# Performance work log

Hardware: AMD Instinct MI355X
Metric: run time of the kernel (lower is better)

The kernel has to match this reference:

```python
import jax, jax.numpy as jnp
import numpy as np

S = 16384   # num src nodes
D = 16384   # num dst nodes
FS = 128    # src feature len
FD = 128    # dst feature len
R = 50.0    # dist threshold (m)
L = 2005.0  # box side so avg degree ~ 32
LN_EPS = 1e-5


def setup_inputs() -> dict:
    rng = np.random.default_rng(0)
    src_pos_np = rng.uniform(0.0, L, (S, 2)).astype(np.float32)
    dst_pos_np = rng.uniform(0.0, L, (D, 2)).astype(np.float32)
    # radius-graph edge construction (data-dependent, done once outside jit)
    es, ed = [], []
    CH = 2048
    for i in range(0, S, CH):
        d = np.linalg.norm(src_pos_np[i:i + CH, None, :] - dst_pos_np[None, :, :], axis=-1)
        si, di = np.nonzero(d <= R)
        es.append((si + i).astype(np.int32))
        ed.append(di.astype(np.int32))
    edge_src_idx = jnp.asarray(np.concatenate(es))
    edge_dst_idx = jnp.asarray(np.concatenate(ed))

    key = jax.random.key(0)
    ks = jax.random.split(key, 12)
    w = lambda k, shape: (jax.random.normal(k, shape, jnp.float32) * 0.02)
    return {
        'src_node_features': jax.random.normal(ks[0], (S, FS), jnp.float32),
        'src_node_pos': jnp.asarray(src_pos_np),
        'dst_node_features': jax.random.normal(ks[1], (D, FD), jnp.float32),
        'dst_node_pos': jnp.asarray(dst_pos_np),
        'src_w': w(ks[2], (FS, FS)), 'src_b': jnp.zeros((FS,), jnp.float32),
        'dst_w': w(ks[3], (FD, FD)), 'dst_b': jnp.zeros((FD,), jnp.float32),
        'dist_w': w(ks[4], (2, FD)), 'dist_b': jnp.zeros((FD,), jnp.float32),
        'edge_w1': w(ks[5], (FS + FD + FD, FD)), 'edge_b1': jnp.zeros((FD,), jnp.float32),
        'edge_w2': w(ks[6], (FD, FD)), 'edge_b2': jnp.zeros((FD,), jnp.float32),
        'ln_g': jnp.ones((FD,), jnp.float32), 'ln_b': jnp.zeros((FD,), jnp.float32),
        'out_w': w(ks[7], (FD, FD)), 'out_b': jnp.zeros((FD,), jnp.float32),
        'edge_src_idx': edge_src_idx,
        'edge_dst_idx': edge_dst_idx,
    }


def reference(src_node_features, src_node_pos, dst_node_features, dst_node_pos,
              src_w, src_b, dst_w, dst_b, dist_w, dist_b,
              edge_w1, edge_b1, edge_w2, edge_b2, ln_g, ln_b, out_w, out_b,
              edge_src_idx, edge_dst_idx):
    # node encoders: Linear + ReLU
    src_enc = jax.nn.relu(src_node_features @ src_w + src_b)   # [S, FS]
    dst_enc = jax.nn.relu(dst_node_features @ dst_w + dst_b)   # [D, FD]
    # gather per-edge
    e_src = src_enc[edge_src_idx]                               # [E, FS]
    e_dst = dst_enc[edge_dst_idx]                               # [E, FD]
    e_dpos = src_node_pos[edge_src_idx] - dst_node_pos[edge_dst_idx]  # [E, 2]
    e_dist = jax.nn.relu(e_dpos @ dist_w + dist_b)              # [E, FD]
    # edge MLP: Linear-ReLU-Linear on concat [E, FS+FD+FD]
    e_in = jnp.concatenate([e_src, e_dist, e_dst], axis=-1)
    e_out = jax.nn.relu(e_in @ edge_w1 + edge_b1) @ edge_w2 + edge_b2  # [E, FD]
    # scatter-add to destination nodes
    agg = dst_enc + jax.ops.segment_sum(e_out, edge_dst_idx, num_segments=D)
    # LayerNorm + ReLU + Linear + residual + ReLU
    mu = jnp.mean(agg, axis=-1, keepdims=True)
    var = jnp.mean(jnp.square(agg - mu), axis=-1, keepdims=True)
    ln = (agg - mu) * jax.lax.rsqrt(var + LN_EPS) * ln_g + ln_b
    h = jax.nn.relu(ln) @ out_w + out_b + dst_node_features
    return jax.nn.relu(h)
```

## Files before the change

kernel.cpp:

```cpp
#include <hip/hip_runtime.h>

typedef unsigned short ushort_t;
typedef unsigned int uint_t;
typedef short bhalf8 __attribute__((ext_vector_type(8)));
typedef float f32x4 __attribute__((ext_vector_type(4)));

__device__ __forceinline__ float b2f(ushort_t u) {
    union { uint_t i; float f; } v; v.i = ((uint_t)u) << 16; return v.f;
}
__device__ __forceinline__ float u2f(uint_t u) {
    union { uint_t i; float f; } v; v.i = u; return v.f;
}
__device__ __forceinline__ ushort_t f2b(float f) {
    union { float f; uint_t i; } v; v.f = f;
    uint_t r = v.i + 0x7fffu + ((v.i >> 16) & 1u);
    return (ushort_t)(r >> 16);
}
__device__ __forceinline__ uint_t f2u(float f) {
    union { float f; uint_t i; } v; v.f = f; return v.i;
}
__device__ __forceinline__ uint_t pack_trunc(float lo, float hi) {
    return (f2u(lo) >> 16) | (f2u(hi) & 0xffff0000u);
}
__device__ __forceinline__ uint_t addpack_trunc(uint_t a, uint_t b) {
    union { uint_t i; float f; } t0, t1, s0, s1;
    t0.i = a << 16;          s0.i = b << 16;
    t1.i = a & 0xffff0000u;  s1.i = b & 0xffff0000u;
    return pack_trunc(t0.f + s0.f, t1.f + s1.f);
}

__global__ __launch_bounds__(256) void prep_kernel(
    const float* __restrict__ wsrc, const float* __restrict__ wdst,
    const float* __restrict__ w2,   const float* __restrict__ wout,
    const float* __restrict__ w1,
    ushort_t* __restrict__ msrc, ushort_t* __restrict__ mdst,
    ushort_t* __restrict__ m2,   ushort_t* __restrict__ mout,
    ushort_t* __restrict__ m1a,  ushort_t* __restrict__ m1b,
    ushort_t* __restrict__ m1c,
    const int* __restrict__ edi, int E, int* __restrict__ deg,
    float* __restrict__ hsum, int countB, int zeroB, int Dn)
{
    int b = blockIdx.x, tid = threadIdx.x;
    if (b < 56) {
        const float* ins[7] = { wsrc, wdst, w2, wout, w1, w1 + 128*128, w1 + 256*128 };
        ushort_t* outs[7]   = { msrc, mdst, m2, mout, m1a, m1b, m1c };
        int mat = b >> 3;
        const float* in = ins[mat];
        ushort_t* out = outs[mat];
        int flat = (b & 7)*256 + tid;
        int nt = flat >> 8, rem = flat & 255;
        int ks = rem >> 6, lane = rem & 63;
        int q = lane >> 4, m = lane & 15;
        #pragma unroll
        for (int j = 0; j < 8; ++j)
            out[flat*8 + j] = f2b(in[(ks*32 + q*8 + j)*128 + nt*16 + m]);
    } else if (b < 56 + countB) {
        int i = (b - 56)*256 + tid;
        if (i < E) atomicAdd(&deg[edi[i]], 1);
    } else {
        int zb = b - 56 - countB;
        float4* h4 = (float4*)hsum;
        int total4 = Dn*32;
        for (int i = zb*256 + tid; i < total4; i += zeroB*256)
            h4[i] = make_float4(0.f, 0.f, 0.f, 0.f);
    }
}

__global__ __launch_bounds__(256) void enc2_kernel(
    const float* __restrict__ src_feat, const float* __restrict__ dst_feat,
    const ushort_t* __restrict__ msrc, const ushort_t* __restrict__ mdst,
    const ushort_t* __restrict__ m1a,  const ushort_t* __restrict__ m1c,
    const float* __restrict__ src_b,   const float* __restrict__ dst_b,
    const float* __restrict__ b1,
    ushort_t* __restrict__ Csrc, ushort_t* __restrict__ Cdst,
    ushort_t* __restrict__ dst_enc,
    const int* __restrict__ deg, int* __restrict__ nxt, int Dn,
    int Sb, int Db)
{
    int tid = threadIdx.x, blk = blockIdx.x;

    if (blk == Sb + Db) {
        __shared__ int sums[256];
        int per = Dn >> 8;
        const int4* d4 = (const int4*)(deg + tid*per);
        int4 v[16]; int s = 0;
        #pragma unroll
        for (int k = 0; k < 16; ++k) { v[k] = d4[k]; s += v[k].x + v[k].y + v[k].z + v[k].w; }
        sums[tid] = s;
        __syncthreads();
        for (int off = 1; off < 256; off <<= 1) {
            int x = (tid >= off) ? sums[tid - off] : 0;
            __syncthreads();
            sums[tid] += x;
            __syncthreads();
        }
        int run = sums[tid] - s;
        int4* n4 = (int4*)(nxt + tid*per);
        #pragma unroll
        for (int k = 0; k < 16; ++k) {
            int4 o;
            o.x = run; run += v[k].x;
            o.y = run; run += v[k].y;
            o.z = run; run += v[k].z;
            o.w = run; run += v[k].w;
            n4[k] = o;
        }
        return;
    }

    __shared__ ushort_t A_l[64*136];
    __shared__ ushort_t E_l[64*136];
    __shared__ float b_l[128];
    __shared__ float b2_l[128];

    const float* A; const ushort_t *W1m, *W2m; const float* bias;
    ushort_t *outC, *outEnc; int rowbase; const float* bias2;
    if (blk < Sb) { A = src_feat; W1m = msrc; W2m = m1a; bias = src_b;
                    outC = Csrc; outEnc = nullptr; rowbase = blk*64; bias2 = nullptr; }
    else          { A = dst_feat; W1m = mdst; W2m = m1c; bias = dst_b;
                    outC = Cdst; outEnc = dst_enc; rowbase = (blk - Sb)*64; bias2 = b1; }

    const float4* A4 = (const float4*)A;
    for (int i = tid; i < 2048; i += 256) {
        int r = i >> 5, c = i & 31;
        float4 v = A4[(size_t)(rowbase + r)*32 + c];
        uint2 u;
        u.x = pack_trunc(v.x, v.y);
        u.y = pack_trunc(v.z, v.w);
        *(uint2*)(A_l + r*136 + c*4) = u;
    }
    if (tid < 128) { b_l[tid] = bias[tid]; b2_l[tid] = bias2 ? bias2[tid] : 0.f; }
    __syncthreads();

    int lane = tid & 63, w = tid >> 6, q = lane >> 4, m = lane & 15;
    const bhalf8* Wv1 = (const bhalf8*)W1m;
    f32x4 acc[4][2] = {};
    #pragma unroll
    for (int ks = 0; ks < 4; ++ks) {
        bhalf8 bf0 = Wv1[((2*w)*4 + ks)*64 + lane];
        bhalf8 bf1 = Wv1[((2*w+1)*4 + ks)*64 + lane];
        #pragma unroll
        for (int mt = 0; mt < 4; ++mt) {
            bhalf8 a = *(const bhalf8*)(A_l + (mt*16 + m)*136 + ks*32 + q*8);
            acc[mt][0] = __builtin_amdgcn_mfma_f32_16x16x32_bf16(a, bf0, acc[mt][0], 0, 0, 0);
            acc[mt][1] = __builtin_amdgcn_mfma_f32_16x16x32_bf16(a, bf1, acc[mt][1], 0, 0, 0);
        }
    }
    #pragma unroll
    for (int mt = 0; mt < 4; ++mt)
    #pragma unroll
    for (int nt = 0; nt < 2; ++nt)
    #pragma unroll
    for (int reg = 0; reg < 4; ++reg) {
        int col = w*32 + nt*16 + m;
        int row = mt*16 + q*4 + reg;
        E_l[row*136 + col] = f2b(fmaxf(acc[mt][nt][reg] + b_l[col], 0.f));
    }
    __syncthreads();

    if (outEnc) {
        for (int i = tid; i < 1024; i += 256) {
            int r = i >> 4, c = i & 15;
            ((uint4*)outEnc)[(size_t)(rowbase + r)*16 + c] = *(const uint4*)(E_l + r*136 + c*8);
        }
    }

    const bhalf8* Wv2 = (const bhalf8*)W2m;
    f32x4 acc2[4][2] = {};
    #pragma unroll
    for (int ks = 0; ks < 4; ++ks) {
        bhalf8 bf0 = Wv2[((2*w)*4 + ks)*64 + lane];
        bhalf8 bf1 = Wv2[((2*w+1)*4 + ks)*64 + lane];
        #pragma unroll
        for (int mt = 0; mt < 4; ++mt) {
            bhalf8 a = *(const bhalf8*)(E_l + (mt*16 + m)*136 + ks*32 + q*8);
            acc2[mt][0] = __builtin_amdgcn_mfma_f32_16x16x32_bf16(a, bf0, acc2[mt][0], 0, 0, 0);
            acc2[mt][1] = __builtin_amdgcn_mfma_f32_16x16x32_bf16(a, bf1, acc2[mt][1], 0, 0, 0);
        }
    }
    #pragma unroll
    for (int mt = 0; mt < 4; ++mt)
    #pragma unroll
    for (int nt = 0; nt < 2; ++nt)
    #pragma unroll
    for (int reg = 0; reg < 4; ++reg) {
        int col = w*32 + nt*16 + m;
        int row = mt*16 + q*4 + reg;
        A_l[row*136 + col] = f2b(acc2[mt][nt][reg] + b2_l[col]);
    }
    __syncthreads();
    for (int i = tid; i < 1024; i += 256) {
        int r = i >> 4, c = i & 15;
        ((uint4*)outC)[(size_t)(rowbase + r)*16 + c] = *(const uint4*)(A_l + r*136 + c*8);
    }
}

__global__ __launch_bounds__(256) void fill_sorted(
    const int* __restrict__ esi, const int* __restrict__ edi, int E,
    int* __restrict__ nxt, int2* __restrict__ spair)
{
    int i = blockIdx.x*256 + threadIdx.x;
    if (i < E) {
        int s = esi[i], d = edi[i];
        int p = atomicAdd(&nxt[d], 1);
        spair[p] = make_int2(s, d);
    }
}

__global__ __launch_bounds__(256, 4) void edge_kernel(
    const ushort_t* __restrict__ Csrc, const ushort_t* __restrict__ Cdst,
    const float* __restrict__ src_pos, const float* __restrict__ dst_pos,
    const int2* __restrict__ spair, int E,
    const ushort_t* __restrict__ w1bm,
    const float* __restrict__ dist_w, const float* __restrict__ dist_b,
    float* __restrict__ hsum)
{
    __shared__ char pool[17408];
    __shared__ ushort_t G[64*136];
    __shared__ int s_l[64], d_l[64], dofs_l[64];
    __shared__ uint_t bndmask[2];
    __shared__ float dx_l[64], dy_l[64];
    __shared__ float dw0_l[128], dw1_l[128], db_l[128];

    ushort_t* X  = (ushort_t*)pool;
    ushort_t* Hc = (ushort_t*)pool;

    int tid = threadIdx.x, blk = blockIdx.x;

    if (tid < 64) {
        int slot = blk*64 + tid;
        int s = 0, d = -1;
        float dx = 0.f, dy = 0.f;
        if (slot < E) {
            int2 pr = spair[slot];
            s = pr.x; d = pr.y;
            float2 sp = ((const float2*)src_pos)[s];
            float2 dp = ((const float2*)dst_pos)[d];
            dx = sp.x - dp.x; dy = sp.y - dp.y;
        }
        s_l[tid] = s; d_l[tid] = d;
        dofs_l[tid] = (d >= 0) ? d*128 : -1;
        dx_l[tid] = dx; dy_l[tid] = dy;
    }
    if (tid < 128) {
        dw0_l[tid] = dist_w[tid];
        dw1_l[tid] = dist_w[128 + tid];
        db_l[tid]  = dist_b[tid];
    }
    __syncthreads();

    if (tid < 64) {
        int d = d_l[tid];
        int dn = (tid < 63) ? d_l[tid + 1] : -2;
        bool bnd = (tid == 31) || (tid == 63) || (dn != d);
        unsigned long long mask = __ballot(bnd);
        if (tid == 0) { bndmask[0] = (uint_t)mask; bndmask[1] = (uint_t)(mask >> 32); }
    }

    const uint4* cs4 = (const uint4*)Csrc;
    const uint4* cd4 = (const uint4*)Cdst;
    #pragma unroll
    for (int k = 0; k < 4; ++k) {
        int i = tid + k*256;
        int r = i >> 4, c = i & 15;
        uint4 a = cs4[(size_t)s_l[r]*16 + c];
        uint4 b = cd4[(size_t)max(d_l[r], 0)*16 + c];
        uint4 u;
        u.x = addpack_trunc(a.x, b.x);
        u.y = addpack_trunc(a.y, b.y);
        u.z = addpack_trunc(a.z, b.z);
        u.w = addpack_trunc(a.w, b.w);
        *(uint4*)(G + r*136 + c*8) = u;
    }
    for (int i = tid; i < 4096; i += 256) {
        int r = i >> 6, j2 = (i & 63)*2;
        float dx = dx_l[r], dy = dy_l[r];
        float v0 = fmaxf(fmaf(dx, dw0_l[j2],   fmaf(dy, dw1_l[j2],   db_l[j2])),   0.f);
        float v1 = fmaxf(fmaf(dx, dw0_l[j2+1], fmaf(dy, dw1_l[j2+1], db_l[j2+1])), 0.f);
        *(uint_t*)(X + r*136 + j2) = pack_trunc(v0, v1);
    }
    __syncthreads();

    int lane = tid & 63, w = tid >> 6, q = lane >> 4, m = lane & 15;
    f32x4 acc[4][2] = {};
    const bhalf8* Wv = (const bhalf8*)w1bm;
    #pragma unroll
    for (int ks = 0; ks < 4; ++ks) {
        bhalf8 bf0 = Wv[((2*w)*4 + ks)*64 + lane];
        bhalf8 bf1 = Wv[((2*w+1)*4 + ks)*64 + lane];
        #pragma unroll
        for (int mt = 0; mt < 4; ++mt) {
            bhalf8 a = *(const bhalf8*)(X + (mt*16 + m)*136 + ks*32 + q*8);
            acc[mt][0] = __builtin_amdgcn_mfma_f32_16x16x32_bf16(a, bf0, acc[mt][0], 0, 0, 0);
            acc[mt][1] = __builtin_amdgcn_mfma_f32_16x16x32_bf16(a, bf1, acc[mt][1], 0, 0, 0);
        }
    }
    __syncthreads();

    #pragma unroll
    for (int mt = 0; mt < 4; ++mt)
    #pragma unroll
    for (int nt = 0; nt < 2; ++nt) {
        int col = w*32 + nt*16 + m;
        int row0 = mt*16 + q*4;
        uint2 u;
        u.x = pack_trunc(acc[mt][nt][0], acc[mt][nt][1]);
        u.y = pack_trunc(acc[mt][nt][2], acc[mt][nt][3]);
        *(uint2*)(Hc + col*68 + row0) = u;
    }
    __syncthreads();

    {
        int j = tid & 127, h = tid >> 7;
        uint_t mask = bndmask[h];
        const ushort_t* Hcol = Hc + j*68 + h*32;
        int rbase = h*32;
        float a = 0.f;
        #pragma unroll
        for (int k8 = 0; k8 < 8; ++k8) {
            uint2 hp = *(const uint2*)(Hcol + k8*4);
            float hv[4];
            hv[0] = u2f(hp.x << 16);
            hv[1] = u2f(hp.x & 0xffff0000u);
            hv[2] = u2f(hp.y << 16);
            hv[3] = u2f(hp.y & 0xffff0000u);
            #pragma unroll
            for (int t = 0; t < 4; ++t) {
                int r = rbase + k8*4 + t;
                float g = b2f(G[r*136 + j]);
                a += fmaxf(hv[t] + g, 0.f);
                if ((mask >> (k8*4 + t)) & 1u) {
                    int ofs = dofs_l[r];
                    if (ofs >= 0) atomicAdd(&hsum[(size_t)ofs + j], a);
                    a = 0.f;
                }
            }
        }
    }
}

__global__ __launch_bounds__(256) void aggfinal_kernel(
    const float* __restrict__ hsum, const ushort_t* __restrict__ w2m,
    const float* __restrict__ b2, const int* __restrict__ deg,
    const ushort_t* __restrict__ dst_enc, const float* __restrict__ ln_g,
    const float* __restrict__ ln_b, const ushort_t* __restrict__ moutm,
    const float* __restrict__ out_b, const float* __restrict__ dst_feat,
    float* __restrict__ out)
{
    __shared__ char buf[64*132*4];
    __shared__ ushort_t act_l[64*136];
    __shared__ float b2_l[128], g_l[128], bl_l[128], ob_l[128];
    __shared__ int deg_l[64];
    __shared__ float ps[64][4], ps2[64][4], mu_l[64], inv_l[64];

    ushort_t* A_l = (ushort_t*)buf;
    float* Y = (float*)buf;
    int tid = threadIdx.x, blk = blockIdx.x;

    const float4* hv = (const float4*)hsum;
    for (int i = tid; i < 1024; i += 256) {
        int r = i >> 4, c = i & 15;
        size_t base = (size_t)(blk*64 + r)*32 + c*2;
        float4 p0 = hv[base], p1 = hv[base + 1];
        uint4 u;
        u.x = pack_trunc(p0.x, p0.y);
        u.y = pack_trunc(p0.z, p0.w);
        u.z = pack_trunc(p1.x, p1.y);
        u.w = pack_trunc(p1.z, p1.w);
        *(uint4*)(A_l + r*136 + c*8) = u;
    }
    if (tid < 128) { b2_l[tid] = b2[tid]; g_l[tid] = ln_g[tid];
                     bl_l[tid] = ln_b[tid]; ob_l[tid] = out_b[tid]; }
    if (tid < 64) deg_l[tid] = deg[blk*64 + tid];
    __syncthreads();

    int lane = tid & 63, w = tid >> 6, q = lane >> 4, m = lane & 15;
    f32x4 acc[4][2] = {};
    const bhalf8* Wv = (const bhalf8*)w2m;
    #pragma unroll
    for (int ks = 0; ks < 4; ++ks) {
        bhalf8 bf0 = Wv[((2*w)*4 + ks)*64 + lane];
        bhalf8 bf1 = Wv[((2*w+1)*4 + ks)*64 + lane];
        #pragma unroll
        for (int mt = 0; mt < 4; ++mt) {
            bhalf8 a = *(const bhalf8*)(A_l + (mt*16 + m)*136 + ks*32 + q*8);
            acc[mt][0] = __builtin_amdgcn_mfma_f32_16x16x32_bf16(a, bf0, acc[mt][0], 0, 0, 0);
            acc[mt][1] = __builtin_amdgcn_mfma_f32_16x16x32_bf16(a, bf1, acc[mt][1], 0, 0, 0);
        }
    }
    __syncthreads();

    #pragma unroll
    for (int mt = 0; mt < 4; ++mt)
    #pragma unroll
    for (int nt = 0; nt < 2; ++nt)
    #pragma unroll
    for (int reg = 0; reg < 4; ++reg) {
        int col = w*32 + nt*16 + m;
        int rowl = mt*16 + q*4 + reg;
        size_t grow = (size_t)blk*64 + rowl;
        float v = acc[mt][nt][reg] + (float)deg_l[rowl]*b2_l[col] + b2f(dst_enc[grow*128 + col]);
        Y[rowl*132 + col] = v;
    }
    __syncthreads();

    {
        int r = tid >> 2, t4 = tid & 3;
        float s = 0.f, s2 = 0.f;
        for (int jj = 0; jj < 32; ++jj) {
            float v = Y[r*132 + t4*32 + jj];
            s += v; s2 += v*v;
        }
        ps[r][t4] = s; ps2[r][t4] = s2;
    }
    __syncthreads();
    if (tid < 64) {
        int r = tid;
        float sum = ps[r][0] + ps[r][1] + ps[r][2] + ps[r][3];
        float sum2 = ps2[r][0] + ps2[r][1] + ps2[r][2] + ps2[r][3];
        float mu = sum / 128.f;
        float var = sum2 / 128.f - mu*mu;
        mu_l[r] = mu;
        inv_l[r] = 1.0f / sqrtf(var + 1e-5f);
    }
    __syncthreads();
    for (int i = tid; i < 4096; i += 256) {
        int r = i >> 6, j2 = (i & 63)*2;
        float v0 = fmaxf((Y[r*132 + j2]   - mu_l[r]) * inv_l[r] * g_l[j2]   + bl_l[j2],   0.f);
        float v1 = fmaxf((Y[r*132 + j2+1] - mu_l[r]) * inv_l[r] * g_l[j2+1] + bl_l[j2+1], 0.f);
        *(uint_t*)(act_l + r*136 + j2) = (uint_t)f2b(v0) | ((uint_t)f2b(v1) << 16);
    }
    __syncthreads();

    f32x4 acc2[4][2] = {};
    const bhalf8* Wo = (const bhalf8*)moutm;
    #pragma unroll
    for (int ks = 0; ks < 4; ++ks) {
        bhalf8 bf0 = Wo[((2*w)*4 + ks)*64 + lane];
        bhalf8 bf1 = Wo[((2*w+1)*4 + ks)*64 + lane];
        #pragma unroll
        for (int mt = 0; mt < 4; ++mt) {
            bhalf8 a = *(const bhalf8*)(act_l + (mt*16 + m)*136 + ks*32 + q*8);
            acc2[mt][0] = __builtin_amdgcn_mfma_f32_16x16x32_bf16(a, bf0, acc2[mt][0], 0, 0, 0);
            acc2[mt][1] = __builtin_amdgcn_mfma_f32_16x16x32_bf16(a, bf1, acc2[mt][1], 0, 0, 0);
        }
    }
    #pragma unroll
    for (int mt = 0; mt < 4; ++mt)
    #pragma unroll
    for (int nt = 0; nt < 2; ++nt)
    #pragma unroll
    for (int reg = 0; reg < 4; ++reg) {
        int col = w*32 + nt*16 + m;
        size_t row = (size_t)blk*64 + mt*16 + q*4 + reg;
        float v = acc2[mt][nt][reg] + ob_l[col] + dst_feat[row*128 + col];
        out[row*128 + col] = fmaxf(v, 0.f);
    }
}

extern "C" void kernel_launch(void* const* d_in, const int* in_sizes, int n_in,
                              void* d_out, int out_size, void* d_ws, size_t ws_size,
                              hipStream_t stream)
{
    const float* src_feat = (const float*)d_in[0];
    const float* src_pos  = (const float*)d_in[1];
    const float* dst_feat = (const float*)d_in[2];
    const float* dst_pos  = (const float*)d_in[3];
    const float* src_w    = (const float*)d_in[4];
    const float* src_b    = (const float*)d_in[5];
    const float* dst_w    = (const float*)d_in[6];
    const float* dst_b    = (const float*)d_in[7];
    const float* dist_w   = (const float*)d_in[8];
    const float* dist_b   = (const float*)d_in[9];
    const float* w1       = (const float*)d_in[10];
    const float* b1       = (const float*)d_in[11];
    const float* w2       = (const float*)d_in[12];
    const float* b2       = (const float*)d_in[13];
    const float* ln_g     = (const float*)d_in[14];
    const float* ln_b     = (const float*)d_in[15];
    const float* out_w    = (const float*)d_in[16];
    const float* out_b    = (const float*)d_in[17];
    const int* esi        = (const int*)d_in[18];
    const int* edi        = (const int*)d_in[19];
    int E = in_sizes[18];
    int S = in_sizes[0] / 128;
    int D = in_sizes[2] / 128;

    char* ws = (char*)d_ws;
    size_t off = 0;
    auto alloc = [&](size_t bytes) { char* p = ws + off; off += (bytes + 511) & ~(size_t)511; return p; };
    ushort_t* Csrc    = (ushort_t*)alloc((size_t)S*128*2);
    ushort_t* Cdst    = (ushort_t*)alloc((size_t)D*128*2);
    ushort_t* dst_enc = (ushort_t*)alloc((size_t)D*128*2);
    float*    hsum    = (float*)   alloc((size_t)D*128*4);
    ushort_t* msrc    = (ushort_t*)alloc(128*128*2);
    ushort_t* mdst    = (ushort_t*)alloc(128*128*2);
    ushort_t* m2      = (ushort_t*)alloc(128*128*2);
    ushort_t* mout    = (ushort_t*)alloc(128*128*2);
    ushort_t* m1a     = (ushort_t*)alloc(128*128*2);
    ushort_t* m1b     = (ushort_t*)alloc(128*128*2);
    ushort_t* m1c     = (ushort_t*)alloc(128*128*2);
    int*      deg     = (int*)     alloc((size_t)D*4);
    int*      nxt     = (int*)     alloc((size_t)D*4);
    int2*     spair   = (int2*)    alloc((size_t)E*8);

    hipMemsetAsync(deg, 0, (size_t)D*4, stream);

    int countB = (E + 255)/256;
    int zeroB = 256;
    prep_kernel<<<56 + countB + zeroB, 256, 0, stream>>>(
        src_w, dst_w, w2, out_w, w1,
        msrc, mdst, m2, mout, m1a, m1b, m1c,
        edi, E, deg, hsum, countB, zeroB, D);

    int Sb = S/64, Db = D/64;
    enc2_kernel<<<Sb + Db + 1, 256, 0, stream>>>(
        src_feat, dst_feat, msrc, mdst, m1a, m1c, src_b, dst_b, b1,
        Csrc, Cdst, dst_enc, deg, nxt, D, Sb, Db);

    fill_sorted<<<(E + 255)/256, 256, 0, stream>>>(esi, edi, E, nxt, spair);

    edge_kernel<<<(E + 63)/64, 256, 0, stream>>>(
        Csrc, Cdst, src_pos, dst_pos, spair, E,
        m1b, dist_w, dist_b, hsum);

    aggfinal_kernel<<<Db, 256, 0, stream>>>(
        hsum, m2, b2, deg, dst_enc, ln_g, ln_b,
        mout, out_b, dst_feat, (float*)d_out);
}
```

Before: 224.6 us.

## Fuse all stages into one cooperative persistent kernel with grid syncs

```diff
diff --git a/kernel.cpp b/kernel.cpp
--- a/kernel.cpp
+++ b/kernel.cpp
@@ -1,4 +1,7 @@
 #include <hip/hip_runtime.h>
+#include <hip/hip_cooperative_groups.h>
+
+namespace cg = cooperative_groups;
 
 typedef unsigned short ushort_t;
 typedef unsigned int uint_t;
@@ -27,6 +30,428 @@
     t0.i = a << 16;          s0.i = b << 16;
     t1.i = a & 0xffff0000u;  s1.i = b & 0xffff0000u;
     return pack_trunc(t0.f + s0.f, t1.f + s1.f);
+}
+
+__global__ __launch_bounds__(256, 3) void gnn_mega(
+    const float* __restrict__ src_feat, const float* __restrict__ dst_feat,
+    const float* __restrict__ src_pos,  const float* __restrict__ dst_pos,
+    const float* __restrict__ wsrc, const float* __restrict__ src_b,
+    const float* __restrict__ wdst, const float* __restrict__ dst_b,
+    const float* __restrict__ dist_w, const float* __restrict__ dist_b,
+    const float* __restrict__ w1, const float* __restrict__ b1,
+    const float* __restrict__ w2g, const float* __restrict__ b2g,
+    const float* __restrict__ ln_g, const float* __restrict__ ln_b,
+    const float* __restrict__ woutg, const float* __restrict__ out_bg,
+    const int* __restrict__ esi, const int* __restrict__ edi, int E,
+    ushort_t* __restrict__ t_src, ushort_t* __restrict__ t_dst,
+    ushort_t* __restrict__ t_w2,  ushort_t* __restrict__ t_out,
+    ushort_t* __restrict__ t_1a,  ushort_t* __restrict__ t_1b,
+    ushort_t* __restrict__ t_1c,
+    ushort_t* __restrict__ Csrc, ushort_t* __restrict__ Cdst,
+    ushort_t* __restrict__ dst_enc,
+    float* __restrict__ hsum, int* __restrict__ deg, int* __restrict__ nxt,
+    int2* __restrict__ spair, float* __restrict__ out, int S, int D)
+{
+    __shared__ __align__(16) char smem[37648];
+    int tid = threadIdx.x, blk = blockIdx.x, nB = gridDim.x;
+    int lane = tid & 63, w = tid >> 6, q = lane >> 4, m = lane & 15;
+    cg::grid_group grid = cg::this_grid();
+
+    if (blk < 56) {
+        const float* ins[7] = { wsrc, wdst, w2g, woutg, w1, w1 + 16384, w1 + 32768 };
+        ushort_t* outs[7]   = { t_src, t_dst, t_w2, t_out, t_1a, t_1b, t_1c };
+        int mat = blk >> 3;
+        int flat = (blk & 7)*256 + tid;
+        int nt = flat >> 8, rem = flat & 255;
+        int ks = rem >> 6, l2 = rem & 63;
+        int qq = l2 >> 4, mm = l2 & 15;
+        const float* in = ins[mat];
+        ushort_t* o = outs[mat];
+        #pragma unroll
+        for (int j = 0; j < 8; ++j)
+            o[flat*8 + j] = f2b(in[(ks*32 + qq*8 + j)*128 + nt*16 + mm]);
+    }
+    for (int i = blk*256 + tid; i < E; i += nB*256) atomicAdd(&deg[edi[i]], 1);
+    {
+        float4 z = make_float4(0.f, 0.f, 0.f, 0.f);
+        float4* h4 = (float4*)hsum;
+        int tot = D*32;
+        for (int i = blk*256 + tid; i < tot; i += nB*256) h4[i] = z;
+    }
+    grid.sync();
+
+    int Sb = S/64, Db = D/64;
+    for (int vb = blk; vb < Sb + Db; vb += nB) {
+        ushort_t* A_l = (ushort_t*)smem;
+        ushort_t* E_l = (ushort_t*)(smem + 17408);
+        float* b_l  = (float*)(smem + 34816);
+        float* pb2  = (float*)(smem + 35328);
+
+        const float* A; const ushort_t *W1m, *W2m; const float* bias; const float* bias2;
+        ushort_t *outC, *outEnc; int rowbase;
+        if (vb < Sb) { A = src_feat; W1m = t_src; W2m = t_1a; bias = src_b;
+                       outC = Csrc; outEnc = nullptr; rowbase = vb*64; bias2 = nullptr; }
+        else         { A = dst_feat; W1m = t_dst; W2m = t_1c; bias = dst_b;
+                       outC = Cdst; outEnc = dst_enc; rowbase = (vb - Sb)*64; bias2 = b1; }
+
+        const float4* A4 = (const float4*)A;
+        for (int i = tid; i < 2048; i += 256) {
+            int r = i >> 5, c = i & 31;
+            float4 v = A4[(size_t)(rowbase + r)*32 + c];
+            uint2 u;
+            u.x = pack_trunc(v.x, v.y);
+            u.y = pack_trunc(v.z, v.w);
+            *(uint2*)(A_l + r*136 + c*4) = u;
+        }
+        if (tid < 128) { b_l[tid] = bias[tid]; pb2[tid] = bias2 ? bias2[tid] : 0.f; }
+        __syncthreads();
+
+        const bhalf8* Wv1 = (const bhalf8*)W1m;
+        f32x4 acc[4][2] = {};
+        #pragma unroll
+        for (int ks = 0; ks < 4; ++ks) {
+            bhalf8 bf0 = Wv1[((2*w)*4 + ks)*64 + lane];
+            bhalf8 bf1 = Wv1[((2*w+1)*4 + ks)*64 + lane];
+            #pragma unroll
+            for (int mt = 0; mt < 4; ++mt) {
+                bhalf8 a = *(const bhalf8*)(A_l + (mt*16 + m)*136 + ks*32 + q*8);
+                acc[mt][0] = __builtin_amdgcn_mfma_f32_16x16x32_bf16(a, bf0, acc[mt][0], 0, 0, 0);
+                acc[mt][1] = __builtin_amdgcn_mfma_f32_16x16x32_bf16(a, bf1, acc[mt][1], 0, 0, 0);
+            }
+        }
+        #pragma unroll
+        for (int mt = 0; mt < 4; ++mt)
+        #pragma unroll
+        for (int nt = 0; nt < 2; ++nt)
+        #pragma unroll
+        for (int reg = 0; reg < 4; ++reg) {
+            int col = w*32 + nt*16 + m;
+            int row = mt*16 + q*4 + reg;
+            E_l[row*136 + col] = f2b(fmaxf(acc[mt][nt][reg] + b_l[col], 0.f));
+        }
+        __syncthreads();
+
+        if (outEnc) {
+            for (int i = tid; i < 1024; i += 256) {
+                int r = i >> 4, c = i & 15;
+                ((uint4*)outEnc)[(size_t)(rowbase + r)*16 + c] = *(const uint4*)(E_l + r*136 + c*8);
+            }
+        }
+
+        const bhalf8* Wv2 = (const bhalf8*)W2m;
+        f32x4 acc2[4][2] = {};
+        #pragma unroll
+        for (int ks = 0; ks < 4; ++ks) {
+            bhalf8 bf0 = Wv2[((2*w)*4 + ks)*64 + lane];
+            bhalf8 bf1 = Wv2[((2*w+1)*4 + ks)*64 + lane];
+            #pragma unroll
+            for (int mt = 0; mt < 4; ++mt) {
+                bhalf8 a = *(const bhalf8*)(E_l + (mt*16 + m)*136 + ks*32 + q*8);
+                acc2[mt][0] = __builtin_amdgcn_mfma_f32_16x16x32_bf16(a, bf0, acc2[mt][0], 0, 0, 0);
+                acc2[mt][1] = __builtin_amdgcn_mfma_f32_16x16x32_bf16(a, bf1, acc2[mt][1], 0, 0, 0);
+            }
+        }
+        #pragma unroll
+        for (int mt = 0; mt < 4; ++mt)
+        #pragma unroll
+        for (int nt = 0; nt < 2; ++nt)
+        #pragma unroll
+        for (int reg = 0; reg < 4; ++reg) {
+            int col = w*32 + nt*16 + m;
+            int row = mt*16 + q*4 + reg;
+            A_l[row*136 + col] = f2b(acc2[mt][nt][reg] + pb2[col]);
+        }
+        __syncthreads();
+        for (int i = tid; i < 1024; i += 256) {
+            int r = i >> 4, c = i & 15;
+            ((uint4*)outC)[(size_t)(rowbase + r)*16 + c] = *(const uint4*)(A_l + r*136 + c*8);
+        }
+        __syncthreads();
+    }
+    if (blk == nB - 1) {
+        int* sums = (int*)(smem + 36608);
+        int per = D >> 8;
+        const int4* d4 = (const int4*)(deg + tid*per);
+        int s = 0;
+        for (int k = 0; k < per/4; ++k) { int4 v = d4[k]; s += v.x + v.y + v.z + v.w; }
+        sums[tid] = s;
+        __syncthreads();
+        for (int off = 1; off < 256; off <<= 1) {
+            int x = (tid >= off) ? sums[tid - off] : 0;
+            __syncthreads();
+            sums[tid] += x;
+            __syncthreads();
+        }
+        int run = sums[tid] - s;
+        int4* n4 = (int4*)(nxt + tid*per);
+        for (int k = 0; k < per/4; ++k) {
+            int4 v = d4[k];
+            int4 o;
+            o.x = run; run += v.x;
+            o.y = run; run += v.y;
+            o.z = run; run += v.z;
+            o.w = run; run += v.w;
+            n4[k] = o;
+        }
+    }
+    grid.sync();
+
+    for (int i = blk*256 + tid; i < E; i += nB*256) {
+        int s = esi[i], d = edi[i];
+        int p = atomicAdd(&nxt[d], 1);
+        spair[p] = make_int2(s, d);
+    }
+    grid.sync();
+
+    {
+        ushort_t* X   = (ushort_t*)smem;
+        ushort_t* G   = (ushort_t*)(smem + 17408);
+        float* dw0    = (float*)(smem + 34816);
+        float* dw1    = (float*)(smem + 35328);
+        float* dbv    = (float*)(smem + 35840);
+        int* s_l      = (int*)(smem + 36352);
+        int* d_l      = (int*)(smem + 36608);
+        int* dofs     = (int*)(smem + 36864);
+        float* dx_l   = (float*)(smem + 37120);
+        float* dy_l   = (float*)(smem + 37376);
+        uint_t* bnd   = (uint_t*)(smem + 37632);
+
+        if (tid < 128) {
+            dw0[tid] = dist_w[tid];
+            dw1[tid] = dist_w[128 + tid];
+            dbv[tid] = dist_b[tid];
+        }
+        const bhalf8* Wv = (const bhalf8*)t_1b;
+        bhalf8 wf0[4], wf1[4];
+        #pragma unroll
+        for (int ks = 0; ks < 4; ++ks) {
+            wf0[ks] = Wv[((2*w)*4 + ks)*64 + lane];
+            wf1[ks] = Wv[((2*w+1)*4 + ks)*64 + lane];
+        }
+
+        int nT = (E + 63) >> 6;
+        for (int tile = blk; tile < nT; tile += nB) {
+            __syncthreads();
+            if (tid < 64) {
+                int slot = tile*64 + tid;
+                int s = 0, d = -1;
+                float dx = 0.f, dy = 0.f;
+                if (slot < E) {
+                    int2 pr = spair[slot];
+                    s = pr.x; d = pr.y;
+                    float2 sp = ((const float2*)src_pos)[s];
+                    float2 dp = ((const float2*)dst_pos)[d];
+                    dx = sp.x - dp.x; dy = sp.y - dp.y;
+                }
+                s_l[tid] = s; d_l[tid] = d;
+                dofs[tid] = (d >= 0) ? d*128 : -1;
+                dx_l[tid] = dx; dy_l[tid] = dy;
+            }
+            __syncthreads();
+            if (tid < 64) {
+                int d = d_l[tid];
+                int dn = (tid < 63) ? d_l[tid + 1] : -2;
+                bool bb = (tid == 31) || (tid == 63) || (dn != d);
+                unsigned long long mask = __ballot(bb);
+                if (tid == 0) { bnd[0] = (uint_t)mask; bnd[1] = (uint_t)(mask >> 32); }
+            }
+            const uint4* cs4 = (const uint4*)Csrc;
+            const uint4* cd4 = (const uint4*)Cdst;
+            #pragma unroll
+            for (int k = 0; k < 4; ++k) {
+                int i = tid + k*256;
+                int r = i >> 4, c = i & 15;
+                uint4 a = cs4[(size_t)s_l[r]*16 + c];
+                uint4 b = cd4[(size_t)max(d_l[r], 0)*16 + c];
+                uint4 u;
+                u.x = addpack_trunc(a.x, b.x);
+                u.y = addpack_trunc(a.y, b.y);
+                u.z = addpack_trunc(a.z, b.z);
+                u.w = addpack_trunc(a.w, b.w);
+                *(uint4*)(G + r*136 + c*8) = u;
+            }
+            for (int i = tid; i < 4096; i += 256) {
+                int r = i >> 6, j2 = (i & 63)*2;
+                float dx = dx_l[r], dy = dy_l[r];
+                float v0 = fmaxf(fmaf(dx, dw0[j2],   fmaf(dy, dw1[j2],   dbv[j2])),   0.f);
+                float v1 = fmaxf(fmaf(dx, dw0[j2+1], fmaf(dy, dw1[j2+1], dbv[j2+1])), 0.f);
+                *(uint_t*)(X + r*136 + j2) = pack_trunc(v0, v1);
+            }
+            __syncthreads();
+
+            f32x4 acc[4][2] = {};
+            #pragma unroll
+            for (int ks = 0; ks < 4; ++ks) {
+                #pragma unroll
+                for (int mt = 0; mt < 4; ++mt) {
+                    bhalf8 a = *(const bhalf8*)(X + (mt*16 + m)*136 + ks*32 + q*8);
+                    acc[mt][0] = __builtin_amdgcn_mfma_f32_16x16x32_bf16(a, wf0[ks], acc[mt][0], 0, 0, 0);
+                    acc[mt][1] = __builtin_amdgcn_mfma_f32_16x16x32_bf16(a, wf1[ks], acc[mt][1], 0, 0, 0);
+                }
+            }
+            __syncthreads();
+
+            ushort_t* Hc = X;
+            #pragma unroll
+            for (int mt = 0; mt < 4; ++mt)
+            #pragma unroll
+            for (int nt = 0; nt < 2; ++nt) {
+                int col = w*32 + nt*16 + m;
+                int row0 = mt*16 + q*4;
+                uint2 u;
+                u.x = pack_trunc(acc[mt][nt][0], acc[mt][nt][1]);
+                u.y = pack_trunc(acc[mt][nt][2], acc[mt][nt][3]);
+                *(uint2*)(Hc + col*68 + row0) = u;
+            }
+            __syncthreads();
+
+            {
+                int j = tid & 127, h = tid >> 7;
+                uint_t mask = bnd[h];
+                const ushort_t* Hcol = Hc + j*68 + h*32;
+                int rbase = h*32;
+                float a = 0.f;
+                #pragma unroll
+                for (int k8 = 0; k8 < 8; ++k8) {
+                    uint2 hp = *(const uint2*)(Hcol + k8*4);
+                    float hv[4];
+                    hv[0] = u2f(hp.x << 16);
+                    hv[1] = u2f(hp.x & 0xffff0000u);
+                    hv[2] = u2f(hp.y << 16);
+                    hv[3] = u2f(hp.y & 0xffff0000u);
+                    #pragma unroll
+                    for (int t = 0; t < 4; ++t) {
+                        int r = rbase + k8*4 + t;
+                        float g = b2f(G[r*136 + j]);
+                        a += fmaxf(hv[t] + g, 0.f);
+                        if ((mask >> (k8*4 + t)) & 1u) {
+                            int ofs = dofs[r];
+                            if (ofs >= 0) atomicAdd(&hsum[(size_t)ofs + j], a);
+                            a = 0.f;
+                        }
+                    }
+                }
+            }
+        }
+    }
+    grid.sync();
+
+    {
+        ushort_t* A_l = (ushort_t*)smem;
+        ushort_t* E2  = (ushort_t*)(smem + 4352);
+        float* ps   = (float*)(smem + 8704);
+        float* ps2  = (float*)(smem + 8960);
+        float* muv  = (float*)(smem + 9216);
+        float* invv = (float*)(smem + 9280);
+        float* pb2  = (float*)(smem + 9344);
+        float* pg   = (float*)(smem + 9856);
+        float* plb  = (float*)(smem + 10368);
+        float* pob  = (float*)(smem + 10880);
+        int*   dgl  = (int*)(smem + 11392);
+
+        int nT4 = D >> 4;
+        for (int t4 = blk; t4 < nT4; t4 += nB) {
+            __syncthreads();
+            if (tid < 128) { pb2[tid] = b2g[tid]; pg[tid] = ln_g[tid];
+                             plb[tid] = ln_b[tid]; pob[tid] = out_bg[tid]; }
+            if (tid < 16) dgl[tid] = deg[t4*16 + tid];
+            {
+                int r = tid >> 4, c = tid & 15;
+                const float4* hv4 = (const float4*)hsum;
+                size_t base = (size_t)(t4*16 + r)*32 + c*2;
+                float4 p0 = hv4[base], p1 = hv4[base + 1];
+                uint4 u;
+                u.x = pack_trunc(p0.x, p0.y);
+                u.y = pack_trunc(p0.z, p0.w);
+                u.z = pack_trunc(p1.x, p1.y);
+                u.w = pack_trunc(p1.z, p1.w);
+                *(uint4*)(A_l + r*136 + c*8) = u;
+                *(uint4*)(E2 + r*136 + c*8) = ((const uint4*)dst_enc)[(size_t)(t4*16 + r)*16 + c];
+            }
+            __syncthreads();
+
+            const bhalf8* Wv2 = (const bhalf8*)t_w2;
+            f32x4 acc[2] = {};
+            #pragma unroll
+            for (int ks = 0; ks < 4; ++ks) {
+                bhalf8 bf0 = Wv2[((2*w)*4 + ks)*64 + lane];
+                bhalf8 bf1 = Wv2[((2*w+1)*4 + ks)*64 + lane];
+                bhalf8 a = *(const bhalf8*)(A_l + m*136 + ks*32 + q*8);
+                acc[0] = __builtin_amdgcn_mfma_f32_16x16x32_bf16(a, bf0, acc[0], 0, 0, 0);
+                acc[1] = __builtin_amdgcn_mfma_f32_16x16x32_bf16(a, bf1, acc[1], 0, 0, 0);
+            }
+            float y[2][4];
+            #pragma unroll
+            for (int nt = 0; nt < 2; ++nt)
+            #pragma unroll
+            for (int reg = 0; reg < 4; ++reg) {
+                int col = w*32 + nt*16 + m;
+                int rowl = q*4 + reg;
+                y[nt][reg] = acc[nt][reg] + (float)dgl[rowl]*pb2[col] + b2f(E2[rowl*136 + col]);
+            }
+            float s[4], s2[4];
+            #pragma unroll
+            for (int reg = 0; reg < 4; ++reg) {
+                s[reg]  = y[0][reg] + y[1][reg];
+                s2[reg] = y[0][reg]*y[0][reg] + y[1][reg]*y[1][reg];
+            }
+            #pragma unroll
+            for (int o = 1; o < 16; o <<= 1) {
+                #pragma unroll
+                for (int reg = 0; reg < 4; ++reg) {
+                    s[reg]  += __shfl_xor(s[reg],  o);
+                    s2[reg] += __shfl_xor(s2[reg], o);
+                }
+            }
+            if (m == 0) {
+                #pragma unroll
+                for (int reg = 0; reg < 4; ++reg) {
+                    ps[(q*4 + reg)*4 + w]  = s[reg];
+                    ps2[(q*4 + reg)*4 + w] = s2[reg];
+                }
+            }
+            __syncthreads();
+            if (tid < 16) {
+                float su = ps[tid*4] + ps[tid*4+1] + ps[tid*4+2] + ps[tid*4+3];
+                float sq = ps2[tid*4] + ps2[tid*4+1] + ps2[tid*4+2] + ps2[tid*4+3];
+                float mu = su / 128.f;
+                float var = sq / 128.f - mu*mu;
+                muv[tid] = mu;
+                invv[tid] = 1.0f / sqrtf(var + 1e-5f);
+            }
+            __syncthreads();
+            #pragma unroll
+            for (int nt = 0; nt < 2; ++nt)
+            #pragma unroll
+            for (int reg = 0; reg < 4; ++reg) {
+                int col = w*32 + nt*16 + m;
+                int rowl = q*4 + reg;
+                float v = (y[nt][reg] - muv[rowl])*invv[rowl]*pg[col] + plb[col];
+                A_l[rowl*136 + col] = f2b(fmaxf(v, 0.f));
+            }
+            __syncthreads();
+
+            const bhalf8* Wo = (const bhalf8*)t_out;
+            f32x4 acc2[2] = {};
+            #pragma unroll
+            for (int ks = 0; ks < 4; ++ks) {
+                bhalf8 bf0 = Wo[((2*w)*4 + ks)*64 + lane];
+                bhalf8 bf1 = Wo[((2*w+1)*4 + ks)*64 + lane];
+                bhalf8 a = *(const bhalf8*)(A_l + m*136 + ks*32 + q*8);
+                acc2[0] = __builtin_amdgcn_mfma_f32_16x16x32_bf16(a, bf0, acc2[0], 0, 0, 0);
+                acc2[1] = __builtin_amdgcn_mfma_f32_16x16x32_bf16(a, bf1, acc2[1], 0, 0, 0);
+            }
+            #pragma unroll
+            for (int nt = 0; nt < 2; ++nt)
+            #pragma unroll
+            for (int reg = 0; reg < 4; ++reg) {
+                int col = w*32 + nt*16 + m;
+                size_t grow = (size_t)t4*16 + q*4 + reg;
+                float v = acc2[nt][reg] + pob[col] + dst_feat[grow*128 + col];
+                out[grow*128 + col] = fmaxf(v, 0.f);
+            }
+        }
+    }
 }
 
 __global__ __launch_bounds__(256) void prep_kernel(
@@ -42,7 +467,7 @@
 {
     int b = blockIdx.x, tid = threadIdx.x;
     if (b < 56) {
-        const float* ins[7] = { wsrc, wdst, w2, wout, w1, w1 + 128*128, w1 + 256*128 };
+        const float* ins[7] = { wsrc, wdst, w2, wout, w1, w1 + 16384, w1 + 32768 };
         ushort_t* outs[7]   = { msrc, mdst, m2, mout, m1a, m1b, m1c };
         int mat = b >> 3;
         const float* in = ins[mat];
@@ -113,8 +538,8 @@
     __shared__ float b_l[128];
     __shared__ float b2_l[128];
 
-    const float* A; const ushort_t *W1m, *W2m; const float* bias;
-    ushort_t *outC, *outEnc; int rowbase; const float* bias2;
+    const float* A; const ushort_t *W1m, *W2m; const float* bias; const float* bias2;
+    ushort_t *outC, *outEnc; int rowbase;
     if (blk < Sb) { A = src_feat; W1m = msrc; W2m = m1a; bias = src_b;
                     outC = Csrc; outEnc = nullptr; rowbase = blk*64; bias2 = nullptr; }
     else          { A = dst_feat; W1m = mdst; W2m = m1c; bias = dst_b;
@@ -493,38 +918,51 @@
     ushort_t* Cdst    = (ushort_t*)alloc((size_t)D*128*2);
     ushort_t* dst_enc = (ushort_t*)alloc((size_t)D*128*2);
     float*    hsum    = (float*)   alloc((size_t)D*128*4);
-    ushort_t* msrc    = (ushort_t*)alloc(128*128*2);
-    ushort_t* mdst    = (ushort_t*)alloc(128*128*2);
-    ushort_t* m2      = (ushort_t*)alloc(128*128*2);
-    ushort_t* mout    = (ushort_t*)alloc(128*128*2);
-    ushort_t* m1a     = (ushort_t*)alloc(128*128*2);
-    ushort_t* m1b     = (ushort_t*)alloc(128*128*2);
-    ushort_t* m1c     = (ushort_t*)alloc(128*128*2);
+    ushort_t* t_src   = (ushort_t*)alloc(128*128*2);
+    ushort_t* t_dst   = (ushort_t*)alloc(128*128*2);
+    ushort_t* t_w2    = (ushort_t*)alloc(128*128*2);
+    ushort_t* t_out   = (ushort_t*)alloc(128*128*2);
+    ushort_t* t_1a    = (ushort_t*)alloc(128*128*2);
+    ushort_t* t_1b    = (ushort_t*)alloc(128*128*2);
+    ushort_t* t_1c    = (ushort_t*)alloc(128*128*2);
     int*      deg     = (int*)     alloc((size_t)D*4);
     int*      nxt     = (int*)     alloc((size_t)D*4);
     int2*     spair   = (int2*)    alloc((size_t)E*8);
+    float*    outp    = (float*)d_out;
 
     hipMemsetAsync(deg, 0, (size_t)D*4, stream);
 
-    int countB = (E + 255)/256;
-    int zeroB = 256;
-    prep_kernel<<<56 + countB + zeroB, 256, 0, stream>>>(
-        src_w, dst_w, w2, out_w, w1,
-        msrc, mdst, m2, mout, m1a, m1b, m1c,
-        edi, E, deg, hsum, countB, zeroB, D);
-
-    int Sb = S/64, Db = D/64;
-    enc2_kernel<<<Sb + Db + 1, 256, 0, stream>>>(
-        src_feat, dst_feat, msrc, mdst, m1a, m1c, src_b, dst_b, b1,
-        Csrc, Cdst, dst_enc, deg, nxt, D, Sb, Db);
-
-    fill_sorted<<<(E + 255)/256, 256, 0, stream>>>(esi, edi, E, nxt, spair);
-
-    edge_kernel<<<(E + 63)/64, 256, 0, stream>>>(
-        Csrc, Cdst, src_pos, dst_pos, spair, E,
-        m1b, dist_w, dist_b, hsum);
-
-    aggfinal_kernel<<<Db, 256, 0, stream>>>(
-        hsum, m2, b2, deg, dst_enc, ln_g, ln_b,
-        mout, out_b, dst_feat, (float*)d_out);
-}
+    void* args[] = {
+        (void*)&src_feat, (void*)&dst_feat, (void*)&src_pos, (void*)&dst_pos,
+        (void*)&src_w, (void*)&src_b, (void*)&dst_w, (void*)&dst_b,
+        (void*)&dist_w, (void*)&dist_b, (void*)&w1, (void*)&b1,
+        (void*)&w2, (void*)&b2, (void*)&ln_g, (void*)&ln_b,
+        (void*)&out_w, (void*)&out_b, (void*)&esi, (void*)&edi, (void*)&E,
+        (void*)&t_src, (void*)&t_dst, (void*)&t_w2, (void*)&t_out,
+        (void*)&t_1a, (void*)&t_1b, (void*)&t_1c,
+        (void*)&Csrc, (void*)&Cdst, (void*)&dst_enc,
+        (void*)&hsum, (void*)&deg, (void*)&nxt, (void*)&spair,
+        (void*)&outp, (void*)&S, (void*)&D
+    };
+    hipError_t rc = hipLaunchCooperativeKernel((void*)gnn_mega, dim3(768), dim3(256),
+                                               args, 0, stream);
+    if (rc != hipSuccess) {
+        int countB = (E + 255)/256;
+        int zeroB = 256;
+        prep_kernel<<<56 + countB + zeroB, 256, 0, stream>>>(
+            src_w, dst_w, w2, out_w, w1,
+            t_src, t_dst, t_w2, t_out, t_1a, t_1b, t_1c,
+            edi, E, deg, hsum, countB, zeroB, D);
+        int Sb = S/64, Db = D/64;
+        enc2_kernel<<<Sb + Db + 1, 256, 0, stream>>>(
+            src_feat, dst_feat, t_src, t_dst, t_1a, t_1c, src_b, dst_b, b1,
+            Csrc, Cdst, dst_enc, deg, nxt, D, Sb, Db);
+        fill_sorted<<<(E + 255)/256, 256, 0, stream>>>(esi, edi, E, nxt, spair);
+        edge_kernel<<<(E + 63)/64, 256, 0, stream>>>(
+            Csrc, Cdst, src_pos, dst_pos, spair, E,
+            t_1b, dist_w, dist_b, hsum);
+        aggfinal_kernel<<<Db, 256, 0, stream>>>(
+            hsum, t_w2, b2, deg, dst_enc, ln_g, ln_b,
+            t_out, out_b, dst_feat, outp);
+    }
+}
```

Result: slower. 623.2 us (+177.5%).

## Shrink final aggregation kernel to 16-row blocks with shuffle-based LayerNorm

Applied to the files above, without the earlier changes.

```diff
diff --git a/kernel.cpp b/kernel.cpp
--- a/kernel.cpp
+++ b/kernel.cpp
@@ -42,7 +42,7 @@
 {
     int b = blockIdx.x, tid = threadIdx.x;
     if (b < 56) {
-        const float* ins[7] = { wsrc, wdst, w2, wout, w1, w1 + 128*128, w1 + 256*128 };
+        const float* ins[7] = { wsrc, wdst, w2, wout, w1, w1 + 16384, w1 + 32768 };
         ushort_t* outs[7]   = { msrc, mdst, m2, mout, m1a, m1b, m1c };
         int mat = b >> 3;
         const float* in = ins[mat];
@@ -113,8 +113,8 @@
     __shared__ float b_l[128];
     __shared__ float b2_l[128];
 
-    const float* A; const ushort_t *W1m, *W2m; const float* bias;
-    ushort_t *outC, *outEnc; int rowbase; const float* bias2;
+    const float* A; const ushort_t *W1m, *W2m; const float* bias; const float* bias2;
+    ushort_t *outC, *outEnc; int rowbase;
     if (blk < Sb) { A = src_feat; W1m = msrc; W2m = m1a; bias = src_b;
                     outC = Csrc; outEnc = nullptr; rowbase = blk*64; bias2 = nullptr; }
     else          { A = dst_feat; W1m = mdst; W2m = m1c; bias = dst_b;
@@ -339,7 +339,7 @@
     }
 }
 
-__global__ __launch_bounds__(256) void aggfinal_kernel(
+__global__ __launch_bounds__(256) void aggfinal16_kernel(
     const float* __restrict__ hsum, const ushort_t* __restrict__ w2m,
     const float* __restrict__ b2, const int* __restrict__ deg,
     const ushort_t* __restrict__ dst_enc, const float* __restrict__ ln_g,
@@ -347,114 +347,113 @@
     const float* __restrict__ out_b, const float* __restrict__ dst_feat,
     float* __restrict__ out)
 {
-    __shared__ char buf[64*132*4];
-    __shared__ ushort_t act_l[64*136];
-    __shared__ float b2_l[128], g_l[128], bl_l[128], ob_l[128];
-    __shared__ int deg_l[64];
-    __shared__ float ps[64][4], ps2[64][4], mu_l[64], inv_l[64];
-
-    ushort_t* A_l = (ushort_t*)buf;
-    float* Y = (float*)buf;
+    __shared__ ushort_t A_l[16*136];
+    __shared__ ushort_t E2[16*136];
+    __shared__ float ps[64], ps2[64];
+    __shared__ float muv[16], invv[16];
+    __shared__ float pb2[128], pg[128], plb[128], pob[128];
+    __shared__ int dgl[16];
+
     int tid = threadIdx.x, blk = blockIdx.x;
-
-    const float4* hv = (const float4*)hsum;
-    for (int i = tid; i < 1024; i += 256) {
-        int r = i >> 4, c = i & 15;
-        size_t base = (size_t)(blk*64 + r)*32 + c*2;
-        float4 p0 = hv[base], p1 = hv[base + 1];
+    int lane = tid & 63, w = tid >> 6, q = lane >> 4, m = lane & 15;
+
+    if (tid < 128) { pb2[tid] = b2[tid]; pg[tid] = ln_g[tid];
+                     plb[tid] = ln_b[tid]; pob[tid] = out_b[tid]; }
+    if (tid < 16) dgl[tid] = deg[blk*16 + tid];
+    {
+        int r = tid >> 4, c = tid & 15;
+        const float4* hv4 = (const float4*)hsum;
+        size_t base = (size_t)(blk*16 + r)*32 + c*2;
+        float4 p0 = hv4[base], p1 = hv4[base + 1];
         uint4 u;
         u.x = pack_trunc(p0.x, p0.y);
         u.y = pack_trunc(p0.z, p0.w);
         u.z = pack_trunc(p1.x, p1.y);
         u.w = pack_trunc(p1.z, p1.w);
         *(uint4*)(A_l + r*136 + c*8) = u;
-    }
-    if (tid < 128) { b2_l[tid] = b2[tid]; g_l[tid] = ln_g[tid];
-                     bl_l[tid] = ln_b[tid]; ob_l[tid] = out_b[tid]; }
-    if (tid < 64) deg_l[tid] = deg[blk*64 + tid];
-    __syncthreads();
-
-    int lane = tid & 63, w = tid >> 6, q = lane >> 4, m = lane & 15;
-    f32x4 acc[4][2] = {};
-    const bhalf8* Wv = (const bhalf8*)w2m;
+        *(uint4*)(E2 + r*136 + c*8) = ((const uint4*)dst_enc)[(size_t)(blk*16 + r)*16 + c];
+    }
+    __syncthreads();
+
+    const bhalf8* Wv2 = (const bhalf8*)w2m;
+    f32x4 acc[2] = {};
     #pragma unroll
     for (int ks = 0; ks < 4; ++ks) {
-        bhalf8 bf0 = Wv[((2*w)*4 + ks)*64 + lane];
-        bhalf8 bf1 = Wv[((2*w+1)*4 + ks)*64 + lane];
-        #pragma unroll
-        for (int mt = 0; mt < 4; ++mt) {
-            bhalf8 a = *(const bhalf8*)(A_l + (mt*16 + m)*136 + ks*32 + q*8);
-            acc[mt][0] = __builtin_amdgcn_mfma_f32_16x16x32_bf16(a, bf0, acc[mt][0], 0, 0, 0);
-            acc[mt][1] = __builtin_amdgcn_mfma_f32_16x16x32_bf16(a, bf1, acc[mt][1], 0, 0, 0);
-        }
-    }
-    __syncthreads();
-
-    #pragma unroll
-    for (int mt = 0; mt < 4; ++mt)
+        bhalf8 bf0 = Wv2[((2*w)*4 + ks)*64 + lane];
+        bhalf8 bf1 = Wv2[((2*w+1)*4 + ks)*64 + lane];
+        bhalf8 a = *(const bhalf8*)(A_l + m*136 + ks*32 + q*8);
+        acc[0] = __builtin_amdgcn_mfma_f32_16x16x32_bf16(a, bf0, acc[0], 0, 0, 0);
+        acc[1] = __builtin_amdgcn_mfma_f32_16x16x32_bf16(a, bf1, acc[1], 0, 0, 0);
+    }
+    float y[2][4];
     #pragma unroll
     for (int nt = 0; nt < 2; ++nt)
     #pragma unroll
     for (int reg = 0; reg < 4; ++reg) {
         int col = w*32 + nt*16 + m;
-        int rowl = mt*16 + q*4 + reg;
-        size_t grow = (size_t)blk*64 + rowl;
-        float v = acc[mt][nt][reg] + (float)deg_l[rowl]*b2_l[col] + b2f(dst_enc[grow*128 + col]);
-        Y[rowl*132 + col] = v;
-    }
-    __syncthreads();
-
-    {
-        int r = tid >> 2, t4 = tid & 3;
-        float s = 0.f, s2 = 0.f;
-        for (int jj = 0; jj < 32; ++jj) {
-            float v = Y[r*132 + t4*32 + jj];
-            s += v; s2 += v*v;
-        }
-        ps[r][t4] = s; ps2[r][t4] = s2;
-    }
-    __syncthreads();
-    if (tid < 64) {
-        int r = tid;
-        float sum = ps[r][0] + ps[r][1] + ps[r][2] + ps[r][3];
-        float sum2 = ps2[r][0] + ps2[r][1] + ps2[r][2] + ps2[r][3];
-        float mu = sum / 128.f;
-        float var = sum2 / 128.f - mu*mu;
-        mu_l[r] = mu;
-        inv_l[r] = 1.0f / sqrtf(var + 1e-5f);
-    }
-    __syncthreads();
-    for (int i = tid; i < 4096; i += 256) {
-        int r = i >> 6, j2 = (i & 63)*2;
-        float v0 = fmaxf((Y[r*132 + j2]   - mu_l[r]) * inv_l[r] * g_l[j2]   + bl_l[j2],   0.f);
-        float v1 = fmaxf((Y[r*132 + j2+1] - mu_l[r]) * inv_l[r] * g_l[j2+1] + bl_l[j2+1], 0.f);
-        *(uint_t*)(act_l + r*136 + j2) = (uint_t)f2b(v0) | ((uint_t)f2b(v1) << 16);
-    }
-    __syncthreads();
-
-    f32x4 acc2[4][2] = {};
+        int rowl = q*4 + reg;
+        y[nt][reg] = acc[nt][reg] + (float)dgl[rowl]*pb2[col] + b2f(E2[rowl*136 + col]);
+    }
+    float s[4], s2[4];
+    #pragma unroll
+    for (int reg = 0; reg < 4; ++reg) {
+        s[reg]  = y[0][reg] + y[1][reg];
+        s2[reg] = y[0][reg]*y[0][reg] + y[1][reg]*y[1][reg];
+    }
+    #pragma unroll
+    for (int o = 1; o < 16; o <<= 1) {
+        #pragma unroll
+        for (int reg = 0; reg < 4; ++reg) {
+            s[reg]  += __shfl_xor(s[reg],  o);
+            s2[reg] += __shfl_xor(s2[reg], o);
+        }
+    }
+    if (m == 0) {
+        #pragma unroll
+        for (int reg = 0; reg < 4; ++reg) {
+            ps[(q*4 + reg)*4 + w]  = s[reg];
+            ps2[(q*4 + reg)*4 + w] = s2[reg];
+        }
+    }
+    __syncthreads();
+    if (tid < 16) {
+        float su = ps[tid*4] + ps[tid*4+1] + ps[tid*4+2] + ps[tid*4+3];
+        float sq = ps2[tid*4] + ps2[tid*4+1] + ps2[tid*4+2] + ps2[tid*4+3];
+        float mu = su / 128.f;
+        float var = sq / 128.f - mu*mu;
+        muv[tid] = mu;
+        invv[tid] = 1.0f / sqrtf(var + 1e-5f);
+    }
+    __syncthreads();
+    #pragma unroll
+    for (int nt = 0; nt < 2; ++nt)
+    #pragma unroll
+    for (int reg = 0; reg < 4; ++reg) {
+        int col = w*32 + nt*16 + m;
+        int rowl = q*4 + reg;
+        float v = (y[nt][reg] - muv[rowl])*invv[rowl]*pg[col] + plb[col];
+        A_l[rowl*136 + col] = f2b(fmaxf(v, 0.f));
+    }
+    __syncthreads();
+
     const bhalf8* Wo = (const bhalf8*)moutm;
+    f32x4 acc2[2] = {};
     #pragma unroll
     for (int ks = 0; ks < 4; ++ks) {
         bhalf8 bf0 = Wo[((2*w)*4 + ks)*64 + lane];
         bhalf8 bf1 = Wo[((2*w+1)*4 + ks)*64 + lane];
-        #pragma unroll
-        for (int mt = 0; mt < 4; ++mt) {
-            bhalf8 a = *(const bhalf8*)(act_l + (mt*16 + m)*136 + ks*32 + q*8);
-            acc2[mt][0] = __builtin_amdgcn_mfma_f32_16x16x32_bf16(a, bf0, acc2[mt][0], 0, 0, 0);
-            acc2[mt][1] = __builtin_amdgcn_mfma_f32_16x16x32_bf16(a, bf1, acc2[mt][1], 0, 0, 0);
-        }
-    }
-    #pragma unroll
-    for (int mt = 0; mt < 4; ++mt)
+        bhalf8 a = *(const bhalf8*)(A_l + m*136 + ks*32 + q*8);
+        acc2[0] = __builtin_amdgcn_mfma_f32_16x16x32_bf16(a, bf0, acc2[0], 0, 0, 0);
+        acc2[1] = __builtin_amdgcn_mfma_f32_16x16x32_bf16(a, bf1, acc2[1], 0, 0, 0);
+    }
     #pragma unroll
     for (int nt = 0; nt < 2; ++nt)
     #pragma unroll
     for (int reg = 0; reg < 4; ++reg) {
         int col = w*32 + nt*16 + m;
-        size_t row = (size_t)blk*64 + mt*16 + q*4 + reg;
-        float v = acc2[mt][nt][reg] + ob_l[col] + dst_feat[row*128 + col];
-        out[row*128 + col] = fmaxf(v, 0.f);
+        size_t grow = (size_t)blk*16 + q*4 + reg;
+        float v = acc2[nt][reg] + pob[col] + dst_feat[grow*128 + col];
+        out[grow*128 + col] = fmaxf(v, 0.f);
     }
 }
 
@@ -493,13 +492,13 @@
     ushort_t* Cdst    = (ushort_t*)alloc((size_t)D*128*2);
     ushort_t* dst_enc = (ushort_t*)alloc((size_t)D*128*2);
     float*    hsum    = (float*)   alloc((size_t)D*128*4);
-    ushort_t* msrc    = (ushort_t*)alloc(128*128*2);
-    ushort_t* mdst    = (ushort_t*)alloc(128*128*2);
-    ushort_t* m2      = (ushort_t*)alloc(128*128*2);
-    ushort_t* mout    = (ushort_t*)alloc(128*128*2);
-    ushort_t* m1a     = (ushort_t*)alloc(128*128*2);
-    ushort_t* m1b     = (ushort_t*)alloc(128*128*2);
-    ushort_t* m1c     = (ushort_t*)alloc(128*128*2);
+    ushort_t* t_src   = (ushort_t*)alloc(128*128*2);
+    ushort_t* t_dst   = (ushort_t*)alloc(128*128*2);
+    ushort_t* t_w2    = (ushort_t*)alloc(128*128*2);
+    ushort_t* t_out   = (ushort_t*)alloc(128*128*2);
+    ushort_t* t_1a    = (ushort_t*)alloc(128*128*2);
+    ushort_t* t_1b    = (ushort_t*)alloc(128*128*2);
+    ushort_t* t_1c    = (ushort_t*)alloc(128*128*2);
     int*      deg     = (int*)     alloc((size_t)D*4);
     int*      nxt     = (int*)     alloc((size_t)D*4);
     int2*     spair   = (int2*)    alloc((size_t)E*8);
@@ -510,21 +509,21 @@
     int zeroB = 256;
     prep_kernel<<<56 + countB + zeroB, 256, 0, stream>>>(
         src_w, dst_w, w2, out_w, w1,
-        msrc, mdst, m2, mout, m1a, m1b, m1c,
+        t_src, t_dst, t_w2, t_out, t_1a, t_1b, t_1c,
         edi, E, deg, hsum, countB, zeroB, D);
 
     int Sb = S/64, Db = D/64;
     enc2_kernel<<<Sb + Db + 1, 256, 0, stream>>>(
-        src_feat, dst_feat, msrc, mdst, m1a, m1c, src_b, dst_b, b1,
+        src_feat, dst_feat, t_src, t_dst, t_1a, t_1c, src_b, dst_b, b1,
         Csrc, Cdst, dst_enc, deg, nxt, D, Sb, Db);
 
     fill_sorted<<<(E + 255)/256, 256, 0, stream>>>(esi, edi, E, nxt, spair);
 
     edge_kernel<<<(E + 63)/64, 256, 0, stream>>>(
         Csrc, Cdst, src_pos, dst_pos, spair, E,
-        m1b, dist_w, dist_b, hsum);
-
-    aggfinal_kernel<<<Db, 256, 0, stream>>>(
-        hsum, m2, b2, deg, dst_enc, ln_g, ln_b,
-        mout, out_b, dst_feat, (float*)d_out);
-}
+        t_1b, dist_w, dist_b, hsum);
+
+    aggfinal16_kernel<<<D/16, 256, 0, stream>>>(
+        hsum, t_w2, b2, deg, dst_enc, ln_g, ln_b,
+        t_out, out_b, dst_feat, (float*)d_out);
+}
```

Measured after the change: 217.2 us. 3.3% less time.
